# Optimization experiments

Measured on AMD Instinct MI355X. Metric: run time of the kernel, lower is better.

The kernel has to match this reference:

```python
import jax, jax.numpy as jnp
import numpy as np

B, T, A = 1024, 64, 6
STOCH, DETER, HIDDEN, EMBED = 30, 200, 200, 1024
RSSM_STD = 0.1


def setup_inputs() -> dict:
    key = jax.random.key(0)
    ks = jax.random.split(key, 20)
    r = lambda k, shape, scale=0.05: (jax.random.normal(k, shape, jnp.float32) * scale)
    inp = {
        'embed': jax.random.normal(ks[0], (B, T, EMBED), jnp.float32),
        'action': jax.random.normal(ks[1], (B, T, A), jnp.float32),
        'noise_prior': jax.random.normal(ks[2], (B, T, STOCH), jnp.float32),
        'noise_post': jax.random.normal(ks[3], (B, T, STOCH), jnp.float32),
        # fc_input: Linear(stoch+A -> hidden)
        'Wi': r(ks[4], (HIDDEN, STOCH + A)), 'bi': jnp.zeros((HIDDEN,), jnp.float32),
        # GRUCell(hidden -> deter)
        'W_ih': r(ks[5], (3 * DETER, HIDDEN)), 'W_hh': r(ks[6], (3 * DETER, DETER)),
        'b_ih': jnp.zeros((3 * DETER,), jnp.float32), 'b_hh': jnp.zeros((3 * DETER,), jnp.float32),
        # fc_prior: Linear(deter->hidden), ELU, Linear(hidden->2*stoch)
        'Wp1': r(ks[7], (HIDDEN, DETER)), 'bp1': jnp.zeros((HIDDEN,), jnp.float32),
        'Wp2': r(ks[8], (2 * STOCH, HIDDEN)), 'bp2': jnp.zeros((2 * STOCH,), jnp.float32),
        # fc_post: Linear(deter+embed->hidden), ELU, Linear(hidden->2*stoch)
        'Wq1': r(ks[9], (HIDDEN, DETER + EMBED)), 'bq1': jnp.zeros((HIDDEN,), jnp.float32),
        'Wq2': r(ks[10], (2 * STOCH, HIDDEN)), 'bq2': jnp.zeros((2 * STOCH,), jnp.float32),
    }
    return inp


def _gru_cell(x, h, W_ih, W_hh, b_ih, b_hh):
    gi = x @ W_ih.T + b_ih  # (B, 3*deter)
    gh = h @ W_hh.T + b_hh
    i_r, i_z, i_n = jnp.split(gi, 3, axis=-1)
    h_r, h_z, h_n = jnp.split(gh, 3, axis=-1)
    r = jax.nn.sigmoid(i_r + h_r)
    z = jax.nn.sigmoid(i_z + h_z)
    n = jnp.tanh(i_n + r * h_n)
    return (1.0 - z) * n + z * h


def reference(embed, action, noise_prior, noise_post,
              Wi, bi, W_ih, W_hh, b_ih, b_hh,
              Wp1, bp1, Wp2, bp2, Wq1, bq1, Wq2, bq2):
    # observe(): scan over time; carry = (post_stoch, deter)
    def step(carry, inp):
        stoch, deter = carry
        a_t, e_t, np_t, nq_t = inp
        # img_step
        x = jax.nn.elu(jnp.concatenate([stoch, a_t], -1) @ Wi.T + bi)
        deter_new = _gru_cell(x, deter, W_ih, W_hh, b_ih, b_hh)
        hp = jax.nn.elu(deter_new @ Wp1.T + bp1)
        pm, ps = jnp.split(hp @ Wp2.T + bp2, 2, axis=-1)
        ps = jax.nn.softplus(ps) + RSSM_STD
        pst = np_t * ps + pm
        # posterior
        hq = jax.nn.elu(jnp.concatenate([deter_new, e_t], -1) @ Wq1.T + bq1)
        qm, qs = jnp.split(hq @ Wq2.T + bq2, 2, axis=-1)
        qs = jax.nn.softplus(qs) + RSSM_STD
        qst = nq_t * qs + qm
        out = jnp.concatenate([qm, qs, qst, deter_new, pm, ps, pst, deter_new], -1)
        return (qst, deter_new), out

    Bsz = action.shape[0]
    init = (jnp.zeros((Bsz, STOCH), action.dtype), jnp.zeros((Bsz, DETER), action.dtype))
    xs = (jnp.swapaxes(action, 0, 1), jnp.swapaxes(embed, 0, 1),
          jnp.swapaxes(noise_prior, 0, 1), jnp.swapaxes(noise_post, 0, 1))
    _, outs = jax.lax.scan(step, init, xs)  # (T, B, 2*(3*stoch+deter))
    # (B, T, 580): [post_mean, post_std, post_stoch, post_deter, prior_mean, prior_std, prior_stoch, prior_deter]
    return jnp.swapaxes(outs, 0, 1)
```

## Files before the change

kernel.cpp:

```cpp
#include <hip/hip_runtime.h>
#include <math.h>

typedef unsigned short u16;
typedef unsigned int   u32;
typedef __attribute__((ext_vector_type(8))) short short8;
typedef __attribute__((ext_vector_type(4))) float f32x4;

#define NBATCH 1024
#define NT 64
#define OC 580
#define RB 16
#define SCAN_BLOCKS (NBATCH / RB)
#define SX 232
#define SF 212

#define P_WI    0
#define P_WIH   26624
#define P_WHH   306176
#define P_WQ1   585728
#define P_WQ2   678912
#define P_EB    707584
#define P_WP1   1133568
#define P_WP2   1226752
#define P_TOTAL 1255424

__device__ __forceinline__ float elu_f(float x) { return x > 0.f ? x : __expf(x) - 1.f; }
__device__ __forceinline__ float sig_f(float x) { return __fdividef(1.f, 1.f + __expf(-x)); }
__device__ __forceinline__ float sp_f(float x)  { return x > 20.f ? x : log1pf(__expf(x)); }
__device__ __forceinline__ float tanh_f(float x) {
    float ax = fabsf(x); ax = ax > 10.f ? 10.f : ax;
    float e = __expf(2.f * ax);
    float t = __fdividef(e - 1.f, e + 1.f);
    return copysignf(t, x);
}

__device__ __forceinline__ void bar_lds() {
    __builtin_amdgcn_sched_barrier(0);
    asm volatile("s_waitcnt lgkmcnt(0)" ::: "memory");
    __builtin_amdgcn_s_barrier();
    __builtin_amdgcn_sched_barrier(0);
}

__device__ __forceinline__ u16 f2b(float f) {
    union { float f; u32 u; } v; v.f = f;
    u32 r = (v.u + 0x7fffu + ((v.u >> 16) & 1u)) >> 16;
    return (u16)r;
}

__device__ __forceinline__ short8 pack8(float4 v0, float4 v1) {
    short8 r;
    r[0] = (short)f2b(v0.x); r[1] = (short)f2b(v0.y);
    r[2] = (short)f2b(v0.z); r[3] = (short)f2b(v0.w);
    r[4] = (short)f2b(v1.x); r[5] = (short)f2b(v1.y);
    r[6] = (short)f2b(v1.z); r[7] = (short)f2b(v1.w);
    return r;
}

#define MFMA(a, b, c) __builtin_amdgcn_mfma_f32_16x16x32_bf16((a), (b), (c), 0, 0, 0)

__global__ __launch_bounds__(256) void prep_pack(
    const float* __restrict__ Wi, const float* __restrict__ W_ih,
    const float* __restrict__ W_hh, const float* __restrict__ Wq1,
    const float* __restrict__ Wq2, const float* __restrict__ Wp1,
    const float* __restrict__ Wp2, u16* __restrict__ wp)
{
    for (size_t r = (size_t)blockIdx.x * 256 + threadIdx.x; r < P_TOTAL;
         r += (size_t)gridDim.x * 256) {
        float val = 0.f;
        if (r < P_WIH) {
            int tile = r / 1024, lane = (r % 1024) / 8, el = r % 8;
            int tt = tile / 2, ks = tile % 2;
            int j = tt * 16 + (lane & 15), k = ks * 32 + (lane >> 4) * 8 + el;
            if (j < 200 && k < 36 && lane < 64) val = Wi[j * 36 + k];
        } else if (r < P_WHH) {
            size_t q = r - P_WIH;
            int tile = q / 1024, lane = (q % 1024) / 8, el = q % 8;
            int g = tile / 91, rem = tile % 91, tt = rem / 7, ks = rem % 7;
            int j = tt * 16 + (lane & 15), k = ks * 32 + (lane >> 4) * 8 + el;
            if (j < 200 && k < 200 && lane < 64) val = W_ih[(size_t)(g * 200 + j) * 200 + k];
        } else if (r < P_WQ1) {
            size_t q = r - P_WHH;
            int tile = q / 1024, lane = (q % 1024) / 8, el = q % 8;
            int g = tile / 91, rem = tile % 91, tt = rem / 7, ks = rem % 7;
            int j = tt * 16 + (lane & 15), k = ks * 32 + (lane >> 4) * 8 + el;
            if (j < 200 && k < 200 && lane < 64) val = W_hh[(size_t)(g * 200 + j) * 200 + k];
        } else if (r < P_WQ2) {
            size_t q = r - P_WQ1;
            int tile = q / 1024, lane = (q % 1024) / 8, el = q % 8;
            int tt = tile / 7, ks = tile % 7;
            int j = tt * 16 + (lane & 15), k = ks * 32 + (lane >> 4) * 8 + el;
            if (j < 200 && k < 200 && lane < 64) val = Wq1[(size_t)j * 1224 + k];
        } else if (r < P_EB) {
            size_t q = r - P_WQ2;
            int tile = q / 1024, lane = (q % 1024) / 8, el = q % 8;
            int tt = tile / 7, ks = tile % 7;
            int j = tt * 16 + (lane & 15), k = ks * 32 + (lane >> 4) * 8 + el;
            if (j < 60 && k < 200 && lane < 64) val = Wq2[(size_t)j * 200 + k];
        } else if (r < P_WP1) {
            size_t q = r - P_EB;
            int tile = q / 1024, lane = (q % 1024) / 8, el = q % 8;
            int ks = tile / 13, tt = tile % 13;
            int j = tt * 16 + (lane & 15), k = ks * 32 + (lane >> 4) * 8 + el;
            if (j < 200 && lane < 64) val = Wq1[(size_t)j * 1224 + 200 + k];
        } else if (r < P_WP2) {
            size_t q = r - P_WP1;
            int tile = q / 1024, lane = (q % 1024) / 8, el = q % 8;
            int ks = tile / 13, tt = tile % 13;
            int j = tt * 16 + (lane & 15), k = ks * 32 + (lane >> 4) * 8 + el;
            if (j < 200 && k < 200 && lane < 64) val = Wp1[(size_t)j * 200 + k];
        } else {
            size_t q = r - P_WP2;
            int tile = q / 1024, lane = (q % 1024) / 8, el = q % 8;
            int ks = tile / 4, tt = tile % 4;
            int j = tt * 16 + (lane & 15), k = ks * 32 + (lane >> 4) * 8 + el;
            if (j < 60 && k < 200 && lane < 64) val = Wp2[(size_t)j * 200 + k];
        }
        wp[r] = f2b(val);
    }
}

__global__ __launch_bounds__(512) void epre_mfma(
    const float* __restrict__ embed, const u16* __restrict__ wp,
    const float* __restrict__ bq1, float* __restrict__ out)
{
    const int tid = threadIdx.x;
    const int wv = tid >> 6, ln = tid & 63;
    const int arow = ln & 15, kgrp = ln >> 4;
    const int m0 = blockIdx.x * 256 + wv * 32;

    f32x4 acc[2][13];
    #pragma unroll
    for (int tt = 0; tt < 13; ++tt) {
        const int j = tt * 16 + arow;
        const float bv = (j < 200) ? bq1[j] : 0.f;
        acc[0][tt] = (f32x4){bv, bv, bv, bv};
        acc[1][tt] = acc[0][tt];
    }
    const float* e0 = &embed[(size_t)(m0 + arow) * 1024 + kgrp * 8];
    const float* e1 = e0 + (size_t)16 * 1024;

    for (int ks = 0; ks < 32; ++ks) {
        short8 a0, a1;
        {
            float4 v0 = *(const float4*)(e0 + ks * 32);
            float4 v1 = *(const float4*)(e0 + ks * 32 + 4);
            a0 = pack8(v0, v1);
            float4 w0 = *(const float4*)(e1 + ks * 32);
            float4 w1 = *(const float4*)(e1 + ks * 32 + 4);
            a1 = pack8(w0, w1);
        }
        const u16* bp = &wp[P_EB + (size_t)ks * 13 * 1024 + (size_t)ln * 8];
        #pragma unroll
        for (int tt = 0; tt < 13; ++tt) {
            short8 b = *(const short8*)(bp + (size_t)tt * 1024);
            acc[0][tt] = MFMA(a0, b, acc[0][tt]);
            acc[1][tt] = MFMA(a1, b, acc[1][tt]);
        }
    }
    #pragma unroll
    for (int f = 0; f < 2; ++f) {
        const size_t rbase = (size_t)(m0 + f * 16 + kgrp * 4);
        #pragma unroll
        for (int tt = 0; tt < 13; ++tt) {
            const int j = tt * 16 + arow;
            if (j < 200) {
                #pragma unroll
                for (int e = 0; e < 4; ++e)
                    out[(rbase + e) * OC + 290 + j] = acc[f][tt][e];
            }
        }
    }
}

__global__ __launch_bounds__(512, 2) void scan_mfma(
    const float* __restrict__ action, const float* __restrict__ noise_post,
    const float* __restrict__ b_ih, const float* __restrict__ b_hh,
    const float* __restrict__ bi, const float* __restrict__ bq2,
    const u16* __restrict__ wp, float* __restrict__ out)
{
    __shared__ u16   s_in0[RB][72];
    __shared__ u16   s_x[RB][SX];
    __shared__ u16   s_db[RB][SX];
    __shared__ u16   s_hq[RB][SX];
    __shared__ float s_df[RB][200];
    __shared__ float s_ep[RB][SF];
    __shared__ float s_r[RB][SF], s_z[RB][SF], s_inn[RB][SF], s_hnn[RB][SF];
    __shared__ float s_q[RB][64];
    __shared__ float s_bih[3][208], s_bhh[3][208], s_bi[208], s_bq2[64];

    const int tid  = threadIdx.x;
    const int wv   = tid >> 6, ln = tid & 63;
    const int arow = ln & 15, kgrp = ln >> 4;
    const int b0   = blockIdx.x * RB;

    { u32* z = (u32*)s_in0; for (int i = tid; i < RB*72/2;  i += 512) z[i] = 0; }
    { u32* z = (u32*)s_x;   for (int i = tid; i < RB*SX/2;  i += 512) z[i] = 0; }
    { u32* z = (u32*)s_db;  for (int i = tid; i < RB*SX/2;  i += 512) z[i] = 0; }
    { u32* z = (u32*)s_hq;  for (int i = tid; i < RB*SX/2;  i += 512) z[i] = 0; }
    { float* z = (float*)s_ep; for (int i = tid; i < RB*SF; i += 512) z[i] = 0.f; }
    { float* z = (float*)s_df; for (int i = tid; i < RB*200; i += 512) z[i] = 0.f; }
    for (int i = tid; i < 3 * 208; i += 512) {
        int g = i / 208, j = i % 208;
        s_bih[g][j] = j < 200 ? b_ih[g * 200 + j] : 0.f;
        s_bhh[g][j] = j < 200 ? b_hh[g * 200 + j] : 0.f;
    }
    for (int i = tid; i < 208; i += 512) s_bi[i] = i < 200 ? bi[i] : 0.f;
    if (tid < 64) s_bq2[tid] = tid < 60 ? bq2[tid] : 0.f;

    short8 whhP[5][7];
    #pragma unroll
    for (int q = 0; q < 5; ++q) {
        int p = wv + 8 * q; int pe = p < 39 ? p : 0;
        #pragma unroll
        for (int ks = 0; ks < 7; ++ks)
            whhP[q][ks] = *(const short8*)&wp[P_WHH + ((size_t)pe * 7 + ks) * 1024 + ln * 8];
    }
    __syncthreads();

    for (int t = 0; t < NT; ++t) {
        for (int idx = tid; idx < RB * 200; idx += 512) {
            int i = idx / 200, j = idx % 200;
            s_ep[i][j] = out[((size_t)(b0 + i) * NT + t) * OC + 290 + j];
        }
        if (tid < RB * 6) {
            int i = tid / 6, c = tid % 6;
            s_in0[i][30 + c] = f2b(action[((size_t)(b0 + i) * NT + t) * 6 + c]);
        }
        bar_lds();

        for (int tt = wv; tt < 13; tt += 8) {
            float bv = s_bi[tt * 16 + arow];
            f32x4 acc = {bv, bv, bv, bv};
            #pragma unroll
            for (int ks = 0; ks < 2; ++ks) {
                short8 af = *(const short8*)&s_in0[arow][ks * 32 + kgrp * 8];
                short8 wf = *(const short8*)&wp[P_WI + (size_t)(tt * 2 + ks) * 1024 + ln * 8];
                acc = MFMA(af, wf, acc);
            }
            #pragma unroll
            for (int e = 0; e < 4; ++e)
                s_x[kgrp * 4 + e][tt * 16 + arow] = f2b(elu_f(acc[e]));
        }
        bar_lds();

        {
            f32x4 gi[5], gh[5];
            #pragma unroll
            for (int q = 0; q < 5; ++q) {
                int p = wv + 8 * q; int pe = p < 39 ? p : 0;
                int g = pe / 13, tt = pe % 13;
                float b1 = s_bih[g][tt * 16 + arow];
                float b2 = s_bhh[g][tt * 16 + arow];
                gi[q] = (f32x4){b1, b1, b1, b1};
                gh[q] = (f32x4){b2, b2, b2, b2};
            }
            #pragma unroll
            for (int ks = 0; ks < 7; ++ks) {
                short8 ax = *(const short8*)&s_x[arow][ks * 32 + kgrp * 8];
                short8 ad = *(const short8*)&s_db[arow][ks * 32 + kgrp * 8];
                #pragma unroll
                for (int q = 0; q < 5; ++q) {
                    int p = wv + 8 * q; int pe = p < 39 ? p : 0;
                    short8 w1 = *(const short8*)&wp[P_WIH + ((size_t)pe * 7 + ks) * 1024 + ln * 8];
                    gi[q] = MFMA(ax, w1, gi[q]);
                    gh[q] = MFMA(ad, whhP[q][ks], gh[q]);
                }
            }
            #pragma unroll
            for (int q = 0; q < 5; ++q) {
                int p = wv + 8 * q;
                if (p < 39) {
                    int g = p / 13, tt = p % 13, j = tt * 16 + arow;
                    #pragma unroll
                    for (int e = 0; e < 4; ++e) {
                        int i = kgrp * 4 + e;
                        if (g == 0)      s_r[i][j] = sig_f(gi[q][e] + gh[q][e]);
                        else if (g == 1) s_z[i][j] = sig_f(gi[q][e] + gh[q][e]);
                        else { s_inn[i][j] = gi[q][e]; s_hnn[i][j] = gh[q][e]; }
                    }
                }
            }
        }
        bar_lds();

        for (int idx = tid; idx < RB * 200; idx += 512) {
            int i = idx / 200, j = idx % 200;
            float rr = s_r[i][j], zz = s_z[i][j];
            float nn = tanh_f(s_inn[i][j] + rr * s_hnn[i][j]);
            float d = (1.f - zz) * nn + zz * s_df[i][j];
            s_df[i][j] = d;
            s_db[i][j] = f2b(d);
            size_t o = ((size_t)(b0 + i) * NT + t) * OC;
            out[o + 90 + j]  = d;
            out[o + 380 + j] = d;
        }
        bar_lds();

        float nz = 0.f;
        if (tid < RB * 30)
            nz = noise_post[((size_t)(b0 + tid / 30) * NT + t) * 30 + (tid % 30)];
        for (int tt = wv; tt < 13; tt += 8) {
            int j = tt * 16 + arow;
            f32x4 acc;
            #pragma unroll
            for (int e = 0; e < 4; ++e) acc[e] = s_ep[kgrp * 4 + e][j];
            for (int ks = 0; ks < 7; ++ks) {
                short8 ad = *(const short8*)&s_db[arow][ks * 32 + kgrp * 8];
                short8 wf = *(const short8*)&wp[P_WQ1 + ((size_t)tt * 7 + ks) * 1024 + ln * 8];
                acc = MFMA(ad, wf, acc);
            }
            #pragma unroll
            for (int e = 0; e < 4; ++e)
                s_hq[kgrp * 4 + e][j] = f2b(elu_f(acc[e]));
        }
        bar_lds();

        if (wv < 4) {
            int tt = wv, j = tt * 16 + arow;
            float bv = s_bq2[j];
            f32x4 acc = {bv, bv, bv, bv};
            for (int ks = 0; ks < 7; ++ks) {
                short8 ah = *(const short8*)&s_hq[arow][ks * 32 + kgrp * 8];
                short8 wf = *(const short8*)&wp[P_WQ2 + ((size_t)tt * 7 + ks) * 1024 + ln * 8];
                acc = MFMA(ah, wf, acc);
            }
            #pragma unroll
            for (int e = 0; e < 4; ++e) s_q[kgrp * 4 + e][j] = acc[e];
        }
        bar_lds();

        if (tid < RB * 30) {
            int i = tid / 30, s = tid % 30;
            float qm = s_q[i][s];
            float qs = sp_f(s_q[i][30 + s]) + 0.1f;
            size_t bt = (size_t)(b0 + i) * NT + t;
            float qst = nz * qs + qm;
            size_t o = bt * OC;
            out[o + s]      = qm;
            out[o + 30 + s] = qs;
            out[o + 60 + s] = qst;
            s_in0[i][s] = f2b(qst);
        }
    }
}

__global__ __launch_bounds__(256) void prior_mfma(
    const float* __restrict__ noise_prior, const u16* __restrict__ wp,
    const float* __restrict__ bp1, const float* __restrict__ bp2,
    float* __restrict__ out)
{
    __shared__ __align__(16) u16   s_hp[64][232];
    __shared__ __align__(16) float s_p[64][68];
    const int tid = threadIdx.x;
    const int wv = tid >> 6, ln = tid & 63;
    const int arow = ln & 15, kgrp = ln >> 4;
    const size_t bt0 = (size_t)blockIdx.x * 64;
    const int m0 = wv * 16;

    for (int idx = tid; idx < 64 * 32; idx += 256) {
        int r2 = idx >> 5, c = 200 + (idx & 31);
        s_hp[r2][c] = 0;
    }

    f32x4 acc[13];
    #pragma unroll
    for (int tt = 0; tt < 13; ++tt) {
        const int j = tt * 16 + arow;
        const float bv = (j < 200) ? bp1[j] : 0.f;
        acc[tt] = (f32x4){bv, bv, bv, bv};
    }
    for (int ks = 0; ks < 7; ++ks) {
        short8 a;
        const int k0 = ks * 32 + kgrp * 8;
        if (k0 <= 192) {
            const float* dp = &out[(bt0 + m0 + arow) * OC + 380 + k0];
            float4 v0 = *(const float4*)dp;
            float4 v1 = *(const float4*)(dp + 4);
            a = pack8(v0, v1);
        } else {
            a = (short8){0, 0, 0, 0, 0, 0, 0, 0};
        }
        const u16* bp = &wp[P_WP1 + (size_t)ks * 13 * 1024 + (size_t)ln * 8];
        #pragma unroll
        for (int tt = 0; tt < 13; ++tt)
            acc[tt] = MFMA(a, *(const short8*)(bp + (size_t)tt * 1024), acc[tt]);
    }
    #pragma unroll
    for (int tt = 0; tt < 13; ++tt)
        #pragma unroll
        for (int e = 0; e < 4; ++e)
            s_hp[m0 + kgrp * 4 + e][tt * 16 + arow] = f2b(elu_f(acc[tt][e]));
    __syncthreads();

    f32x4 acc2[4];
    #pragma unroll
    for (int tt = 0; tt < 4; ++tt) {
        const int j = tt * 16 + arow;
        const float bv = (j < 60) ? bp2[j] : 0.f;
        acc2[tt] = (f32x4){bv, bv, bv, bv};
    }
    #pragma unroll
    for (int ks = 0; ks < 7; ++ks) {
        short8 ah = *(const short8*)&s_hp[m0 + arow][ks * 32 + kgrp * 8];
        const u16* bp = &wp[P_WP2 + (size_t)ks * 4 * 1024 + (size_t)ln * 8];
        #pragma unroll
        for (int tt = 0; tt < 4; ++tt)
            acc2[tt] = MFMA(ah, *(const short8*)(bp + (size_t)tt * 1024), acc2[tt]);
    }
    #pragma unroll
    for (int tt = 0; tt < 4; ++tt)
        #pragma unroll
        for (int e = 0; e < 4; ++e)
            s_p[m0 + kgrp * 4 + e][tt * 16 + arow] = acc2[tt][e];
    __syncthreads();

    for (int idx = tid; idx < 64 * 30; idx += 256) {
        int i = idx / 30, ss = idx - i * 30;
        float pm = s_p[i][ss];
        float ps = sp_f(s_p[i][30 + ss]) + 0.1f;
        float pst = noise_prior[(bt0 + i) * 30 + ss] * ps + pm;
        size_t base = (bt0 + i) * OC;
        out[base + 290 + ss] = pm;
        out[base + 320 + ss] = ps;
        out[base + 350 + ss] = pst;
    }
}

extern "C" void kernel_launch(void* const* d_in, const int* in_sizes, int n_in,
                              void* d_out, int out_size, void* d_ws, size_t ws_size,
                              hipStream_t stream)
{
    (void)in_sizes; (void)n_in; (void)out_size; (void)ws_size;
    const float* embed       = (const float*)d_in[0];
    const float* action      = (const float*)d_in[1];
    const float* noise_prior = (const float*)d_in[2];
    const float* noise_post  = (const float*)d_in[3];
    const float* Wi   = (const float*)d_in[4];
    const float* bi   = (const float*)d_in[5];
    const float* W_ih = (const float*)d_in[6];
    const float* W_hh = (const float*)d_in[7];
    const float* b_ih = (const float*)d_in[8];
    const float* b_hh = (const float*)d_in[9];
    const float* Wp1  = (const float*)d_in[10];
    const float* bp1  = (const float*)d_in[11];
    const float* Wp2  = (const float*)d_in[12];
    const float* bp2  = (const float*)d_in[13];
    const float* Wq1  = (const float*)d_in[14];
    const float* bq1  = (const float*)d_in[15];
    const float* Wq2  = (const float*)d_in[16];
    const float* bq2  = (const float*)d_in[17];
    float* out = (float*)d_out;
    u16* wp = (u16*)d_ws;

    hipLaunchKernelGGL(prep_pack, dim3((P_TOTAL + 255) / 256), dim3(256), 0, stream,
                       Wi, W_ih, W_hh, Wq1, Wq2, Wp1, Wp2, wp);
    hipLaunchKernelGGL(epre_mfma, dim3(256), dim3(512), 0, stream,
                       embed, wp, bq1, out);
    hipLaunchKernelGGL(scan_mfma, dim3(SCAN_BLOCKS), dim3(512), 0, stream,
                       action, noise_post, b_ih, b_hh, bi, bq2, wp, out);
    hipLaunchKernelGGL(prior_mfma, dim3(NBATCH * NT / 64), dim3(256), 0, stream,
                       noise_prior, wp, bp1, bp2, out);
}
```

Before: 1.239 ms.

## Double scan block to 1024 threads and stream W_hh instead of keeping it in registers

Raises the recurrent scan kernel from 8 to 16 waves per block, so each wave handles at most 3 gate tiles instead of 5, and the input and posterior MLP tiles map one per wave. The register-resident W_hh fragments are dropped; W_hh is now read from global memory every timestep alongside W_ih, with base addresses and biases hoisted out of the time loop. The aim is more parallelism per serial timestep on only 64 blocks, at the cost of more weight traffic per step and heavier barrier synchronization with 16 waves.

```diff
diff --git a/kernel.cpp b/kernel.cpp
--- a/kernel.cpp
+++ b/kernel.cpp
@@ -11,6 +11,7 @@
 #define OC 580
 #define RB 16
 #define SCAN_BLOCKS (NBATCH / RB)
+#define NTH 1024
 #define SX 232
 #define SF 212
 
@@ -172,7 +173,7 @@
     }
 }
 
-__global__ __launch_bounds__(512, 2) void scan_mfma(
+__global__ __launch_bounds__(NTH, 4) void scan_mfma(
     const float* __restrict__ action, const float* __restrict__ noise_post,
     const float* __restrict__ b_ih, const float* __restrict__ b_hh,
     const float* __restrict__ bi, const float* __restrict__ bq2,
@@ -193,32 +194,40 @@
     const int arow = ln & 15, kgrp = ln >> 4;
     const int b0   = blockIdx.x * RB;
 
-    { u32* z = (u32*)s_in0; for (int i = tid; i < RB*72/2;  i += 512) z[i] = 0; }
-    { u32* z = (u32*)s_x;   for (int i = tid; i < RB*SX/2;  i += 512) z[i] = 0; }
-    { u32* z = (u32*)s_db;  for (int i = tid; i < RB*SX/2;  i += 512) z[i] = 0; }
-    { u32* z = (u32*)s_hq;  for (int i = tid; i < RB*SX/2;  i += 512) z[i] = 0; }
-    { float* z = (float*)s_ep; for (int i = tid; i < RB*SF; i += 512) z[i] = 0.f; }
-    { float* z = (float*)s_df; for (int i = tid; i < RB*200; i += 512) z[i] = 0.f; }
-    for (int i = tid; i < 3 * 208; i += 512) {
+    { u32* z = (u32*)s_in0; for (int i = tid; i < RB*72/2;  i += NTH) z[i] = 0; }
+    { u32* z = (u32*)s_x;   for (int i = tid; i < RB*SX/2;  i += NTH) z[i] = 0; }
+    { u32* z = (u32*)s_db;  for (int i = tid; i < RB*SX/2;  i += NTH) z[i] = 0; }
+    { u32* z = (u32*)s_hq;  for (int i = tid; i < RB*SX/2;  i += NTH) z[i] = 0; }
+    { float* z = (float*)s_ep; for (int i = tid; i < RB*SF; i += NTH) z[i] = 0.f; }
+    { float* z = (float*)s_df; for (int i = tid; i < RB*200; i += NTH) z[i] = 0.f; }
+    for (int i = tid; i < 3 * 208; i += NTH) {
         int g = i / 208, j = i % 208;
         s_bih[g][j] = j < 200 ? b_ih[g * 200 + j] : 0.f;
         s_bhh[g][j] = j < 200 ? b_hh[g * 200 + j] : 0.f;
     }
-    for (int i = tid; i < 208; i += 512) s_bi[i] = i < 200 ? bi[i] : 0.f;
+    for (int i = tid; i < 208; i += NTH) s_bi[i] = i < 200 ? bi[i] : 0.f;
     if (tid < 64) s_bq2[tid] = tid < 60 ? bq2[tid] : 0.f;
-
-    short8 whhP[5][7];
-    #pragma unroll
-    for (int q = 0; q < 5; ++q) {
-        int p = wv + 8 * q; int pe = p < 39 ? p : 0;
-        #pragma unroll
-        for (int ks = 0; ks < 7; ++ks)
-            whhP[q][ks] = *(const short8*)&wp[P_WHH + ((size_t)pe * 7 + ks) * 1024 + ln * 8];
-    }
     __syncthreads();
 
+    bool uv[3]; int ug[3], uj[3]; size_t bI[3], bH[3]; float sbi[3], sbh[3];
+    #pragma unroll
+    for (int q = 0; q < 3; ++q) {
+        int u = wv + 16 * q;
+        uv[q] = (u < 39);
+        int pe = uv[q] ? u : 0;
+        int g = pe / 13, tt = pe % 13;
+        ug[q] = g; uj[q] = tt * 16 + arow;
+        sbi[q] = s_bih[g][uj[q]];
+        sbh[q] = s_bhh[g][uj[q]];
+        bI[q] = P_WIH + ((size_t)pe * 7) * 1024 + (size_t)ln * 8;
+        bH[q] = P_WHH + ((size_t)pe * 7) * 1024 + (size_t)ln * 8;
+    }
+    const bool hasA = (wv < 13);
+    const int  tA   = hasA ? wv : 0;
+    const int  jA   = tA * 16 + arow;
+
     for (int t = 0; t < NT; ++t) {
-        for (int idx = tid; idx < RB * 200; idx += 512) {
+        for (int idx = tid; idx < RB * 200; idx += NTH) {
             int i = idx / 200, j = idx % 200;
             s_ep[i][j] = out[((size_t)(b0 + i) * NT + t) * OC + 290 + j];
         }
@@ -228,54 +237,51 @@
         }
         bar_lds();
 
-        for (int tt = wv; tt < 13; tt += 8) {
-            float bv = s_bi[tt * 16 + arow];
+        if (hasA) {
+            float bv = s_bi[jA];
             f32x4 acc = {bv, bv, bv, bv};
             #pragma unroll
             for (int ks = 0; ks < 2; ++ks) {
                 short8 af = *(const short8*)&s_in0[arow][ks * 32 + kgrp * 8];
-                short8 wf = *(const short8*)&wp[P_WI + (size_t)(tt * 2 + ks) * 1024 + ln * 8];
+                short8 wf = *(const short8*)&wp[P_WI + (size_t)(tA * 2 + ks) * 1024 + ln * 8];
                 acc = MFMA(af, wf, acc);
             }
             #pragma unroll
             for (int e = 0; e < 4; ++e)
-                s_x[kgrp * 4 + e][tt * 16 + arow] = f2b(elu_f(acc[e]));
+                s_x[kgrp * 4 + e][jA] = f2b(elu_f(acc[e]));
         }
         bar_lds();
 
         {
-            f32x4 gi[5], gh[5];
-            #pragma unroll
-            for (int q = 0; q < 5; ++q) {
-                int p = wv + 8 * q; int pe = p < 39 ? p : 0;
-                int g = pe / 13, tt = pe % 13;
-                float b1 = s_bih[g][tt * 16 + arow];
-                float b2 = s_bhh[g][tt * 16 + arow];
-                gi[q] = (f32x4){b1, b1, b1, b1};
-                gh[q] = (f32x4){b2, b2, b2, b2};
+            f32x4 gi[3], gh[3];
+            #pragma unroll
+            for (int q = 0; q < 3; ++q) {
+                gi[q] = (f32x4){sbi[q], sbi[q], sbi[q], sbi[q]};
+                gh[q] = (f32x4){sbh[q], sbh[q], sbh[q], sbh[q]};
             }
             #pragma unroll
             for (int ks = 0; ks < 7; ++ks) {
                 short8 ax = *(const short8*)&s_x[arow][ks * 32 + kgrp * 8];
                 short8 ad = *(const short8*)&s_db[arow][ks * 32 + kgrp * 8];
                 #pragma unroll
-                for (int q = 0; q < 5; ++q) {
-                    int p = wv + 8 * q; int pe = p < 39 ? p : 0;
-                    short8 w1 = *(const short8*)&wp[P_WIH + ((size_t)pe * 7 + ks) * 1024 + ln * 8];
-                    gi[q] = MFMA(ax, w1, gi[q]);
-                    gh[q] = MFMA(ad, whhP[q][ks], gh[q]);
+                for (int q = 0; q < 3; ++q) {
+                    if (uv[q]) {
+                        short8 w1 = *(const short8*)&wp[bI[q] + (size_t)ks * 1024];
+                        short8 w2 = *(const short8*)&wp[bH[q] + (size_t)ks * 1024];
+                        gi[q] = MFMA(ax, w1, gi[q]);
+                        gh[q] = MFMA(ad, w2, gh[q]);
+                    }
                 }
             }
             #pragma unroll
-            for (int q = 0; q < 5; ++q) {
-                int p = wv + 8 * q;
-                if (p < 39) {
-                    int g = p / 13, tt = p % 13, j = tt * 16 + arow;
+            for (int q = 0; q < 3; ++q) {
+                if (uv[q]) {
+                    const int j = uj[q];
                     #pragma unroll
                     for (int e = 0; e < 4; ++e) {
                         int i = kgrp * 4 + e;
-                        if (g == 0)      s_r[i][j] = sig_f(gi[q][e] + gh[q][e]);
-                        else if (g == 1) s_z[i][j] = sig_f(gi[q][e] + gh[q][e]);
+                        if (ug[q] == 0)      s_r[i][j] = sig_f(gi[q][e] + gh[q][e]);
+                        else if (ug[q] == 1) s_z[i][j] = sig_f(gi[q][e] + gh[q][e]);
                         else { s_inn[i][j] = gi[q][e]; s_hnn[i][j] = gh[q][e]; }
                     }
                 }
@@ -283,7 +289,7 @@
         }
         bar_lds();
 
-        for (int idx = tid; idx < RB * 200; idx += 512) {
+        for (int idx = tid; idx < RB * 200; idx += NTH) {
             int i = idx / 200, j = idx % 200;
             float rr = s_r[i][j], zz = s_z[i][j];
             float nn = tanh_f(s_inn[i][j] + rr * s_hnn[i][j]);
@@ -299,19 +305,18 @@
         float nz = 0.f;
         if (tid < RB * 30)
             nz = noise_post[((size_t)(b0 + tid / 30) * NT + t) * 30 + (tid % 30)];
-        for (int tt = wv; tt < 13; tt += 8) {
-            int j = tt * 16 + arow;
+        if (hasA) {
             f32x4 acc;
             #pragma unroll
-            for (int e = 0; e < 4; ++e) acc[e] = s_ep[kgrp * 4 + e][j];
+            for (int e = 0; e < 4; ++e) acc[e] = s_ep[kgrp * 4 + e][jA];
             for (int ks = 0; ks < 7; ++ks) {
                 short8 ad = *(const short8*)&s_db[arow][ks * 32 + kgrp * 8];
-                short8 wf = *(const short8*)&wp[P_WQ1 + ((size_t)tt * 7 + ks) * 1024 + ln * 8];
+                short8 wf = *(const short8*)&wp[P_WQ1 + ((size_t)tA * 7 + ks) * 1024 + ln * 8];
                 acc = MFMA(ad, wf, acc);
             }
             #pragma unroll
             for (int e = 0; e < 4; ++e)
-                s_hq[kgrp * 4 + e][j] = f2b(elu_f(acc[e]));
+                s_hq[kgrp * 4 + e][jA] = f2b(elu_f(acc[e]));
         }
         bar_lds();
 
@@ -456,7 +461,7 @@
                        Wi, W_ih, W_hh, Wq1, Wq2, Wp1, Wp2, wp);
     hipLaunchKernelGGL(epre_mfma, dim3(256), dim3(512), 0, stream,
                        embed, wp, bq1, out);
-    hipLaunchKernelGGL(scan_mfma, dim3(SCAN_BLOCKS), dim3(512), 0, stream,
+    hipLaunchKernelGGL(scan_mfma, dim3(SCAN_BLOCKS), dim3(NTH), 0, stream,
                        action, noise_post, b_ih, b_hh, bi, bq2, wp, out);
     hipLaunchKernelGGL(prior_mfma, dim3(NBATCH * NT / 64), dim3(256), 0, stream,
                        noise_prior, wp, bp1, bp2, out);
```

Result: slower. 1.390 ms (+12.2%).
